# Kernel tuning notes

Hardware: AMD Instinct MI355X
Metric: run time of the kernel (lower is better)

Reference implementation:

```python
import jax, jax.numpy as jnp
import numpy as np

D_MODEL = 512
NHEAD = 8
HEAD_DIM = D_MODEL // NHEAD
D_FF = 2048
EPS = 1e-5


def _linear_params(key, d_in, d_out):
    kw, kb = jax.random.split(key)
    bound = 1.0 / np.sqrt(d_in)
    W = jax.random.uniform(kw, (d_out, d_in), jnp.float32, -bound, bound)
    b = jax.random.uniform(kb, (d_out,), jnp.float32, -bound, bound)
    return W, b


def setup_inputs() -> dict:
    key = jax.random.key(0)
    ks = jax.random.split(key, 8)
    src = jax.random.normal(ks[0], (4, 2048, D_MODEL), jnp.float32)
    Wq, bq = _linear_params(ks[1], D_MODEL, D_MODEL)
    Wk, bk = _linear_params(ks[2], D_MODEL, D_MODEL)
    Wv, bv = _linear_params(ks[3], D_MODEL, D_MODEL)
    Wo, bo = _linear_params(ks[4], D_MODEL, D_MODEL)
    W1, b1 = _linear_params(ks[5], D_MODEL, D_FF)
    W2, b2 = _linear_params(ks[6], D_FF, D_MODEL)
    g1 = jnp.ones((D_MODEL,), jnp.float32)
    be1 = jnp.zeros((D_MODEL,), jnp.float32)
    g2 = jnp.ones((D_MODEL,), jnp.float32)
    be2 = jnp.zeros((D_MODEL,), jnp.float32)
    return dict(src=src, Wq=Wq, bq=bq, Wk=Wk, bk=bk, Wv=Wv, bv=bv,
                Wo=Wo, bo=bo, W1=W1, b1=b1, W2=W2, b2=b2,
                g1=g1, be1=be1, g2=g2, be2=be2)


def _layer_norm(x, g, b):
    mu = jnp.mean(x, axis=-1, keepdims=True)
    var = jnp.mean(jnp.square(x - mu), axis=-1, keepdims=True)
    return (x - mu) / jnp.sqrt(var + EPS) * g + b


def reference(src, Wq, bq, Wk, bk, Wv, bv, Wo, bo, W1, b1, W2, b2, g1, be1, g2, be2):
    B, T, D = src.shape
    scale = np.sqrt(HEAD_DIM).astype(np.float32)
    # Projections (torch Linear: x @ W.T + b)
    Q = (src @ Wq.T + bq).reshape(B, T, NHEAD, HEAD_DIM).transpose(0, 2, 1, 3)
    K = (src @ Wk.T + bk).reshape(B, T, NHEAD, HEAD_DIM).transpose(0, 2, 1, 3)
    V = (src @ Wv.T + bv).reshape(B, T, NHEAD, HEAD_DIM).transpose(0, 2, 1, 3)
    # Explicit QK^T -> softmax -> V (no mask, dropout=0)
    scores = jnp.einsum('bhqd,bhkd->bhqk', Q, K) / scale  # (B,H,T,T)
    attn = jax.nn.softmax(scores, axis=-1)
    ctx = jnp.einsum('bhqk,bhkd->bhqd', attn, V)
    ctx = ctx.transpose(0, 2, 1, 3).reshape(B, T, D)
    attn_out = ctx @ Wo.T + bo
    # Add & Norm 1
    x = _layer_norm(src + attn_out, g1, be1)
    # FFN: Linear -> GELU -> Linear
    h = jax.nn.gelu(x @ W1.T + b1, approximate=False)
    ffn_out = h @ W2.T + b2
    # Add & Norm 2
    return _layer_norm(x + ffn_out, g2, be2)
```

## Files before the change

### kernel.cpp

```cpp
#include <hip/hip_runtime.h>
#include <hip/hip_bf16.h>
#include <hip/hip_fp16.h>
#include <math.h>

typedef __bf16 bf16_t;
typedef __bf16 bf16x8 __attribute__((ext_vector_type(8)));
typedef __bf16 bf16x2 __attribute__((ext_vector_type(2)));
typedef float  f32x4  __attribute__((ext_vector_type(4)));

#define D_MODEL 512
#define NHEAD   8
#define HD      64
#define D_FF    2048
#define TOKENS  8192
#define SEQ     2048
#define BATCH   4

__device__ __forceinline__ void gload16(const bf16_t* g, bf16_t* l)
{
    __builtin_amdgcn_global_load_lds(
        (const __attribute__((address_space(1))) void*)g,
        (__attribute__((address_space(3))) void*)l,
        16, 0, 0);
}

__device__ __forceinline__ void cvt4(const float* s, bf16_t* d)
{
    float4 v = *(const float4*)s;
    alignas(8) bf16_t t[4] = {(bf16_t)v.x, (bf16_t)v.y, (bf16_t)v.z, (bf16_t)v.w};
    *(uint2*)d = *(const uint2*)t;
}

__device__ __forceinline__ void barrier_raw() { asm volatile("s_barrier" ::: "memory"); }
__device__ __forceinline__ void sched_fence() { __builtin_amdgcn_sched_barrier(0); }

__device__ __forceinline__ float gelu_f(float x)
{
    const float y = fabsf(x) * 0.70710678118654752f;
    const float t = 1.0f / fmaf(0.3275911f, y, 1.0f);
    float p = fmaf(1.061405429f, t, -1.453152027f);
    p = fmaf(p, t, 1.421413741f);
    p = fmaf(p, t, -0.284496736f);
    p = fmaf(p, t, 0.254829592f);
    p *= t;
    const float e = __builtin_amdgcn_exp2f(-y * y * 1.4426950408889634f);
    float erfv = 1.0f - p * e;
    erfv = (x < 0.f) ? -erfv : erfv;
    return 0.5f * x * (1.0f + erfv);
}

__global__ void cvt_weights(const float* __restrict__ src,
                            const float* __restrict__ Wq, const float* __restrict__ Wk,
                            const float* __restrict__ Wv, const float* __restrict__ Wo,
                            const float* __restrict__ W1, const float* __restrict__ W2,
                            const float* __restrict__ bq, const float* __restrict__ bk,
                            const float* __restrict__ bv,
                            bf16_t* __restrict__ Xb,
                            bf16_t* __restrict__ Wqkvb, bf16_t* __restrict__ Wob,
                            bf16_t* __restrict__ W1b, bf16_t* __restrict__ W2b,
                            float* __restrict__ bqkv, float* __restrict__ zbias)
{
    int i = blockIdx.x * 256 + threadIdx.x;
    if (i < 1048576) { cvt4(src + (size_t)i * 4, Xb + (size_t)i * 4); return; }
    i -= 1048576;
    if (i < 65536)        cvt4(Wq + (size_t)i * 4,            Wqkvb + (size_t)i * 4);
    else if (i < 131072)  cvt4(Wk + (size_t)(i - 65536) * 4,  Wqkvb + (size_t)i * 4);
    else if (i < 196608)  cvt4(Wv + (size_t)(i - 131072) * 4, Wqkvb + (size_t)i * 4);
    else if (i < 262144)  cvt4(Wo + (size_t)(i - 196608) * 4, Wob + (size_t)(i - 196608) * 4);
    else if (i < 524288)  cvt4(W1 + (size_t)(i - 262144) * 4, W1b + (size_t)(i - 262144) * 4);
    else if (i < 786432)  cvt4(W2 + (size_t)(i - 524288) * 4, W2b + (size_t)(i - 524288) * 4);
    else if (i < 786816) {
        int j = i - 786432;
        const float* s = (j < 128) ? bq + j * 4 : (j < 256) ? bk + (j - 128) * 4
                                                            : bv + (j - 256) * 4;
        *(float4*)(bqkv + (j & 127) * 4 + (j >> 7) * 512) = *(const float4*)s;
    } else if (i < 786944) {
        int j = i - 786816;
        *(float4*)(zbias + j * 4) = make_float4(0.f, 0.f, 0.f, 0.f);
    }
}

template <int EPI>
__global__ __launch_bounds__(512, 2)
void gemm256(const bf16_t* __restrict__ A, const bf16_t* __restrict__ B,
             const float* __restrict__ bias, bf16_t* __restrict__ C,
             int M, int N, int K)
{
    __shared__ bf16_t sA[2][256][64];
    __shared__ bf16_t sB[2][256][64];
    bf16_t* sAf = &sA[0][0][0];
    bf16_t* sBf = &sB[0][0][0];

    const int tid  = threadIdx.x;
    const int wave = tid >> 6;
    const int lane = tid & 63;
    const int g    = lane >> 4;
    const int c16  = lane & 15;
    const int wm   = (wave >> 2) * 128;
    const int wn   = (wave & 3) * 64;

    const int nwg  = gridDim.x * gridDim.y;
    const int flat = blockIdx.y * gridDim.x + blockIdx.x;
    const int swz  = (flat & 7) * (nwg >> 3) + (flat >> 3);
    const int m0   = (swz / gridDim.x) * 256;
    const int n0   = (swz % gridDim.x) * 256;

    const f32x4 fz = {0.f, 0.f, 0.f, 0.f};
    f32x4 acc[8][4];
#pragma unroll
    for (int i = 0; i < 8; i++)
#pragma unroll
        for (int j = 0; j < 4; j++) acc[i][j] = fz;

    const bf16_t* gA[4]; const bf16_t* gB[4]; int fa[4];
#pragma unroll
    for (int i = 0; i < 4; i++) {
        const int f = i * 512 + tid, row = f >> 3, l = (f & 7) ^ (row & 7);
        fa[i] = f;
        gA[i] = A + (size_t)(m0 + row) * K + l * 8;
        gB[i] = B + (size_t)(n0 + row) * K + l * 8;
    }

    auto stage = [&](int ko, int buf) {
        bf16_t* dA = sAf + buf * (256 * 64);
        bf16_t* dB = sBf + buf * (256 * 64);
#pragma unroll
        for (int i = 0; i < 4; i++) gload16(gA[i] + ko, dA + fa[i] * 8);
#pragma unroll
        for (int i = 0; i < 4; i++) gload16(gB[i] + ko, dB + fa[i] * 8);
    };

    stage(0, 0);
    stage(64, 1);

    const int NS = K >> 6;
    for (int s = 0; s < NS; ++s) {
        const int cur = s & 1;
        if (s + 1 < NS) asm volatile("s_waitcnt vmcnt(8)" ::: "memory");
        else            asm volatile("s_waitcnt vmcnt(0)" ::: "memory");
        barrier_raw();
        sched_fence();

#pragma unroll
        for (int ks = 0; ks < 2; ++ks) {
            const int ck = ((ks * 4 + g) ^ (c16 & 7)) * 8;
            bf16x8 af[8], bfr[4];
#pragma unroll
            for (int i = 0; i < 8; i++)
                af[i] = *(const bf16x8*)&sA[cur][wm + i * 16 + c16][ck];
#pragma unroll
            for (int j = 0; j < 4; j++)
                bfr[j] = *(const bf16x8*)&sB[cur][wn + j * 16 + c16][ck];
#pragma unroll
            for (int mi = 0; mi < 8; mi++)
#pragma unroll
                for (int ni = 0; ni < 4; ni++)
                    acc[mi][ni] = __builtin_amdgcn_mfma_f32_16x16x32_bf16(
                        af[mi], bfr[ni], acc[mi][ni], 0, 0, 0);
        }

        sched_fence();
        barrier_raw();
        if (s + 2 < NS) stage((s + 2) << 6, cur);
        sched_fence();
    }

    float bcol[4];
#pragma unroll
    for (int ni = 0; ni < 4; ni++) bcol[ni] = bias[n0 + wn + ni * 16 + c16];
#pragma unroll
    for (int mi = 0; mi < 8; mi++) {
#pragma unroll
        for (int ni = 0; ni < 4; ni++) {
            const int col = n0 + wn + ni * 16 + c16;
#pragma unroll
            for (int r = 0; r < 4; r++) {
                const int row = m0 + wm + mi * 16 + g * 4 + r;
                float v = acc[mi][ni][r] + bcol[ni];
                if (EPI == 1) v = gelu_f(v);
                C[(size_t)row * N + col] = (bf16_t)v;
            }
        }
    }
}

template <int BM, int EPI, bool SPLIT2>
__global__ __launch_bounds__(256)
void gemm_bt(const bf16_t* __restrict__ A, const bf16_t* __restrict__ B,
             const float* __restrict__ bias, const float* __restrict__ biasz,
             void* __restrict__ Cout, int M, int N, int K)
{
    constexpr int MI = BM / 32;
    constexpr int NA = BM / 32;
    __shared__ bf16_t sA[2][BM][64];
    __shared__ bf16_t sB[2][128][64];
    bf16_t* sAf = &sA[0][0][0];
    bf16_t* sBf = &sB[0][0][0];

    const int tid  = threadIdx.x;
    const int wave = tid >> 6;
    const int lane = tid & 63;
    const int g    = lane >> 4;
    const int c16  = lane & 15;
    const int wm   = (wave >> 1) * (BM / 2);
    const int wn   = (wave & 1) * 64;
    const int m0   = blockIdx.y * BM;
    const int n0   = blockIdx.x * 128;

    const int zz    = SPLIT2 ? blockIdx.z : 0;
    const int Keff  = SPLIT2 ? (K >> 1) : K;
    const int kbase = zz * Keff;
    const float* bptr = (SPLIT2 && zz) ? biasz : bias;

    const f32x4 fz = {0.f, 0.f, 0.f, 0.f};
    f32x4 acc[MI][4];
#pragma unroll
    for (int i = 0; i < MI; i++)
#pragma unroll
        for (int j = 0; j < 4; j++) acc[i][j] = fz;

    const bf16_t* gA[NA]; int fa[NA];
#pragma unroll
    for (int i = 0; i < NA; i++) {
        const int f = i * 256 + tid, row = f >> 3, l = (f & 7) ^ (row & 7);
        fa[i] = f;
        gA[i] = A + (size_t)(m0 + row) * K + kbase + l * 8;
    }
    const bf16_t* gB[4]; int fb[4];
#pragma unroll
    for (int i = 0; i < 4; i++) {
        const int f = i * 256 + tid, row = f >> 3, l = (f & 7) ^ (row & 7);
        fb[i] = f;
        gB[i] = B + (size_t)(n0 + row) * K + kbase + l * 8;
    }

    auto stage = [&](int ko, int buf) {
        bf16_t* dA = sAf + buf * (BM * 64);
        bf16_t* dB = sBf + buf * 8192;
#pragma unroll
        for (int i = 0; i < NA; i++) gload16(gA[i] + ko, dA + fa[i] * 8);
#pragma unroll
        for (int i = 0; i < 4; i++)  gload16(gB[i] + ko, dB + fb[i] * 8);
    };

    stage(0, 0);
    stage(64, 1);

    const int NS = Keff >> 6;
    for (int s = 0; s < NS; ++s) {
        const int cur = s & 1;
        if (s + 1 < NS) {
            if constexpr (NA == 2) asm volatile("s_waitcnt vmcnt(6)" ::: "memory");
            else                   asm volatile("s_waitcnt vmcnt(8)" ::: "memory");
        } else {
            asm volatile("s_waitcnt vmcnt(0)" ::: "memory");
        }
        barrier_raw();
        sched_fence();

#pragma unroll
        for (int sub = 0; sub < 2; ++sub) {
            const int ck = (((sub * 4 + g) ^ (c16 & 7))) * 8;
            bf16x8 af[MI], bfr[4];
#pragma unroll
            for (int i = 0; i < MI; i++)
                af[i] = *(const bf16x8*)&sA[cur][wm + i * 16 + c16][ck];
#pragma unroll
            for (int j = 0; j < 4; j++)
                bfr[j] = *(const bf16x8*)&sB[cur][wn + j * 16 + c16][ck];
#pragma unroll
            for (int mi = 0; mi < MI; mi++)
#pragma unroll
                for (int ni = 0; ni < 4; ni++)
                    acc[mi][ni] = __builtin_amdgcn_mfma_f32_16x16x32_bf16(
                        af[mi], bfr[ni], acc[mi][ni], 0, 0, 0);
        }

        sched_fence();
        barrier_raw();
        if (s + 2 < NS) stage((s + 2) << 6, cur);
        sched_fence();
    }

    __half* outh = (__half*)Cout + (size_t)zz * M * N;
#pragma unroll
    for (int mi = 0; mi < MI; mi++) {
#pragma unroll
        for (int ni = 0; ni < 4; ni++) {
            const int col = n0 + wn + ni * 16 + c16;
            const float bv = bptr[col];
#pragma unroll
            for (int r = 0; r < 4; r++) {
                const int row = m0 + wm + mi * 16 + g * 4 + r;
                float v = acc[mi][ni][r] + bv;
                if (EPI == 1) v = gelu_f(v);
                if (EPI == 2)
                    outh[(size_t)row * N + col] = (__half)v;
                else
                    ((bf16_t*)Cout)[(size_t)row * N + col] = (bf16_t)v;
            }
        }
    }
}

__global__ __launch_bounds__(256)
void transpose_v(const bf16_t* __restrict__ qkv, bf16_t* __restrict__ vt)
{
    __shared__ bf16_t st[64][72];
    const int t0 = blockIdx.x * 64;
    const int bh = blockIdx.y;
    const int b = bh >> 3, h = bh & 7;
    const int tid = threadIdx.x;

    for (int c = tid; c < 512; c += 256) {
        int r = c >> 3, cj = (c & 7) * 8;
        const bf16_t* src = qkv + ((size_t)(b * SEQ + t0 + r)) * 1536 + 1024 + h * 64 + cj;
        *(int4*)&st[r][cj] = *(const int4*)src;
    }
    __syncthreads();
    for (int c = tid; c < 512; c += 256) {
        int d = c >> 3, pj = (c & 7) * 8;
        alignas(16) bf16_t tmp[8];
#pragma unroll
        for (int j = 0; j < 8; j++) {
            int p = pj + j;
            int t = ((p >> 5) << 5) + (((p >> 2) & 1) << 4) + (((p >> 3) & 3) << 2) + (p & 3);
            tmp[j] = st[t][d];
        }
        *(int4*)(vt + ((size_t)(bh * 64 + d)) * SEQ + t0 + pj) = *(const int4*)tmp;
    }
}

__global__ __launch_bounds__(512)
__attribute__((amdgpu_waves_per_eu(6)))
void flash_attn(const bf16_t* __restrict__ qkv, const bf16_t* __restrict__ vt,
                bf16_t* __restrict__ ctx)
{
    __shared__ bf16_t sK[3][64][64];
    __shared__ bf16_t sVt[3][64][64];

    const int bh = blockIdx.y;
    const int b = bh >> 3, h = bh & 7;
    const int q0 = blockIdx.x * 128;
    const int tid = threadIdx.x;
    const int wave = tid >> 6, lane = tid & 63;
    const int g = lane >> 4, c16 = lane & 15;

    const float qscale = 0.125f * 1.4426950408889634f;
    bf16x8 aq[2];
#pragma unroll
    for (int ks = 0; ks < 2; ks++) {
        bf16x8 v = *(const bf16x8*)(qkv +
            ((size_t)(b * SEQ + q0 + wave * 16 + c16)) * 1536 +
            h * 64 + ks * 32 + g * 8);
#pragma unroll
        for (int j = 0; j < 8; j++) v[j] = (bf16_t)((float)v[j] * qscale);
        aq[ks] = v;
    }

    const f32x4 fz = {0.f, 0.f, 0.f, 0.f};
    f32x4 acc_oT[4];
#pragma unroll
    for (int dt = 0; dt < 4; dt++) acc_oT[dt] = fz;
    float l_acc = 0.f;

    const int f0 = tid, r0 = f0 >> 3, l0 = (f0 & 7) ^ (r0 & 7);
    const bf16_t* gK0 = qkv + ((size_t)(b * SEQ + r0)) * 1536 + 512 + h * 64 + l0 * 8;
    const bf16_t* gV0 = vt + ((size_t)(bh * 64 + r0)) * SEQ + l0 * 8;
    bf16_t* lK = &sK[0][0][0];
    bf16_t* lV = &sVt[0][0][0];

    auto stageKV = [&](int t) {
        const int bo = (t % 3) * 4096;
        const size_t kv = (size_t)t * 64;
        gload16(gK0 + kv * 1536, lK + bo + f0 * 8);
        gload16(gV0 + kv,        lV + bo + f0 * 8);
    };

    f32x4 accs[4];
    auto qk_mfma = [&](int cur) {
#pragma unroll
        for (int tt = 0; tt < 4; tt++) accs[tt] = fz;
#pragma unroll
        for (int ks = 0; ks < 2; ks++) {
            const int pc = ((ks * 4 + g) ^ (c16 & 7)) * 8;
#pragma unroll
            for (int tt = 0; tt < 4; tt++) {
                bf16x8 ak = *(const bf16x8*)&sK[cur][tt * 16 + c16][pc];
                accs[tt] = __builtin_amdgcn_mfma_f32_16x16x32_bf16(ak, aq[ks], accs[tt], 0, 0, 0);
            }
        }
    };

    bf16x8 pb[2];
    auto pv_mfma = [&](int cur) {
#pragma unroll
        for (int kv = 0; kv < 2; kv++) {
            const int pc = ((kv * 4 + g) ^ (c16 & 7)) * 8;
#pragma unroll
            for (int dt = 0; dt < 4; dt++) {
                bf16x8 av = *(const bf16x8*)&sVt[cur][dt * 16 + c16][pc];
                acc_oT[dt] = __builtin_amdgcn_mfma_f32_16x16x32_bf16(av, pb[kv], acc_oT[dt], 0, 0, 0);
            }
        }
    };

    auto softmax_pack = [&]() {
#pragma unroll
        for (int tt = 0; tt < 4; tt++) {
            float s = 0.f;
#pragma unroll
            for (int r = 0; r < 4; r++) {
                float p = __builtin_amdgcn_exp2f(accs[tt][r]);
                accs[tt][r] = p;
                s += p;
            }
            l_acc += s;
        }
#pragma unroll
        for (int kv = 0; kv < 2; kv++)
#pragma unroll
            for (int j = 0; j < 8; j++)
                pb[kv][j] = (bf16_t)accs[kv * 2 + (j >> 2)][j & 3];
    };

    stageKV(0);
    stageKV(1);

    for (int it = 0; it < 32; ++it) {
        const int cur = it % 3;
        if (it < 31) asm volatile("s_waitcnt vmcnt(2)" ::: "memory");
        else         asm volatile("s_waitcnt vmcnt(0)" ::: "memory");
        barrier_raw();

        __builtin_amdgcn_s_setprio(1);
        qk_mfma(cur);
        __builtin_amdgcn_s_setprio(0);
        softmax_pack();
        __builtin_amdgcn_s_setprio(1);
        pv_mfma(cur);
        __builtin_amdgcn_s_setprio(0);

        if (it + 2 < 32) stageKV(it + 2);
    }

    {
        float l = l_acc;
        l += __shfl_xor(l, 16);
        l += __shfl_xor(l, 32);
        const float inv = 1.0f / l;
        const int token = q0 + wave * 16 + c16;
        bf16_t* dst = ctx + ((size_t)(b * SEQ + token)) * 512 + h * 64 + g * 4;
#pragma unroll
        for (int dt = 0; dt < 4; dt++) {
            alignas(8) bf16_t o4[4];
#pragma unroll
            for (int r = 0; r < 4; r++) o4[r] = (bf16_t)(acc_oT[dt][r] * inv);
            *(uint2*)(dst + dt * 16) = *(const uint2*)o4;
        }
    }
}

__global__ __launch_bounds__(256)
void add_ln3(const float* __restrict__ a, const __half* __restrict__ b,
             const __half* __restrict__ c,
             const float* __restrict__ gamma, const float* __restrict__ beta,
             float* __restrict__ outf, bf16_t* __restrict__ outb)
{
    const int row  = blockIdx.x * 4 + (threadIdx.x >> 6);
    const int lane = threadIdx.x & 63;
    const size_t base = (size_t)row * 512 + lane * 8;

    int4 braw = *(const int4*)(b + base);
    int4 craw = *(const int4*)(c + base);
    const __half* bh = (const __half*)&braw;
    const __half* ch = (const __half*)&craw;

    float v[8];
#pragma unroll
    for (int hh = 0; hh < 2; hh++) {
        float4 av = *(const float4*)(a + base + hh * 4);
        v[hh * 4 + 0] = av.x + (float)bh[hh * 4 + 0] + (float)ch[hh * 4 + 0];
        v[hh * 4 + 1] = av.y + (float)bh[hh * 4 + 1] + (float)ch[hh * 4 + 1];
        v[hh * 4 + 2] = av.z + (float)bh[hh * 4 + 2] + (float)ch[hh * 4 + 2];
        v[hh * 4 + 3] = av.w + (float)bh[hh * 4 + 3] + (float)ch[hh * 4 + 3];
    }

    float s = 0.f;
#pragma unroll
    for (int i = 0; i < 8; i++) s += v[i];
#pragma unroll
    for (int off = 32; off > 0; off >>= 1) s += __shfl_xor(s, off);
    const float mu = s * (1.f / 512.f);

    float q = 0.f;
#pragma unroll
    for (int i = 0; i < 8; i++) { float d = v[i] - mu; q += d * d; }
#pragma unroll
    for (int off = 32; off > 0; off >>= 1) q += __shfl_xor(q, off);
    const float rstd = rsqrtf(q * (1.f / 512.f) + 1e-5f);

    float4 g0 = *(const float4*)(gamma + lane * 8);
    float4 g1 = *(const float4*)(gamma + lane * 8 + 4);
    float4 e0 = *(const float4*)(beta + lane * 8);
    float4 e1 = *(const float4*)(beta + lane * 8 + 4);
    const float gg[8] = {g0.x, g0.y, g0.z, g0.w, g1.x, g1.y, g1.z, g1.w};
    const float ee[8] = {e0.x, e0.y, e0.z, e0.w, e1.x, e1.y, e1.z, e1.w};

    float o[8];
#pragma unroll
    for (int i = 0; i < 8; i++) o[i] = (v[i] - mu) * rstd * gg[i] + ee[i];

    *(float4*)(outf + base)     = make_float4(o[0], o[1], o[2], o[3]);
    *(float4*)(outf + base + 4) = make_float4(o[4], o[5], o[6], o[7]);
    if (outb) {
        alignas(16) bf16_t ob[8];
#pragma unroll
        for (int i = 0; i < 8; i++) ob[i] = (bf16_t)o[i];
        *(int4*)(outb + base) = *(const int4*)ob;
    }
}

extern "C" void kernel_launch(void* const* d_in, const int* in_sizes, int n_in,
                              void* d_out, int out_size, void* d_ws, size_t ws_size,
                              hipStream_t stream)
{
    const float* src = (const float*)d_in[0];
    const float* Wq  = (const float*)d_in[1];  const float* bq  = (const float*)d_in[2];
    const float* Wk  = (const float*)d_in[3];  const float* bk  = (const float*)d_in[4];
    const float* Wv  = (const float*)d_in[5];  const float* bv  = (const float*)d_in[6];
    const float* Wo  = (const float*)d_in[7];  const float* bo  = (const float*)d_in[8];
    const float* W1  = (const float*)d_in[9];  const float* b1  = (const float*)d_in[10];
    const float* W2  = (const float*)d_in[11]; const float* b2  = (const float*)d_in[12];
    const float* g1  = (const float*)d_in[13]; const float* be1 = (const float*)d_in[14];
    const float* g2  = (const float*)d_in[15]; const float* be2 = (const float*)d_in[16];
    float* out = (float*)d_out;

    char* ws = (char*)d_ws;
    size_t off = 0;
    auto alloc = [&](size_t bytes) -> void* {
        void* p = ws + off;
        off = (off + bytes + 255) & ~(size_t)255;
        return p;
    };

    bf16_t* Xb    = (bf16_t*)alloc((size_t)TOKENS * 512 * 2);
    bf16_t* Wqkvb = (bf16_t*)alloc((size_t)1536 * 512 * 2);
    bf16_t* Wob   = (bf16_t*)alloc((size_t)512 * 512 * 2);
    bf16_t* W1b   = (bf16_t*)alloc((size_t)2048 * 512 * 2);
    bf16_t* W2b   = (bf16_t*)alloc((size_t)512 * 2048 * 2);
    float*  bqkv  = (float*)alloc(1536 * 4);
    float*  zbias = (float*)alloc(512 * 4);
    bf16_t* QKV   = (bf16_t*)alloc((size_t)TOKENS * 1536 * 2);
    bf16_t* Vt    = (bf16_t*)alloc((size_t)32 * 64 * SEQ * 2);
    bf16_t* CTX   = (bf16_t*)alloc((size_t)TOKENS * 512 * 2);
    __half* ATTa  = (__half*)alloc((size_t)TOKENS * 512 * 2);
    __half* ATTb  = (__half*)alloc((size_t)TOKENS * 512 * 2);
    float*  X1    = (float*)alloc((size_t)TOKENS * 512 * 4);
    bf16_t* X1b   = (bf16_t*)alloc((size_t)TOKENS * 512 * 2);

    bf16_t* H    = QKV;
    __half* FFNa = ATTa;
    __half* FFNb = ATTb;

    cvt_weights<<<7170, 256, 0, stream>>>(src, Wq, Wk, Wv, Wo, W1, W2, bq, bk, bv,
                                          Xb, Wqkvb, Wob, W1b, W2b, bqkv, zbias);

    gemm256<0><<<dim3(6, 32), 512, 0, stream>>>(
        Xb, Wqkvb, bqkv, QKV, TOKENS, 1536, 512);

    transpose_v<<<dim3(32, 32), 256, 0, stream>>>(QKV, Vt);
    flash_attn<<<dim3(16, 32), 512, 0, stream>>>(QKV, Vt, CTX);

    gemm_bt<64, 2, true><<<dim3(4, 128, 2), 256, 0, stream>>>(
        CTX, Wob, bo, zbias, ATTa, TOKENS, 512, 512);

    add_ln3<<<2048, 256, 0, stream>>>(src, ATTa, ATTb, g1, be1, X1, X1b);

    gemm_bt<128, 1, false><<<dim3(16, 64), 256, 0, stream>>>(
        X1b, W1b, b1, zbias, H, TOKENS, 2048, 512);

    gemm_bt<64, 2, true><<<dim3(4, 128, 2), 256, 0, stream>>>(
        H, W2b, b2, zbias, FFNa, TOKENS, 512, 2048);

    add_ln3<<<2048, 256, 0, stream>>>(X1, FFNa, FFNb, g2, be2, out, nullptr);
}
```

Before: 269.5 us.

## Fuse V transpose into QKV GEMM epilogue and drop 256-tile GEMM

The QKV projection now runs through the generic 128x128 gemm_bt kernel with a new epilogue mode. In that mode, V columns are written directly into the permuted, transposed Vt layout that flash attention expects. This removes the separate transpose_v kernel launch and its extra read and write of V. In exchange, the dedicated 256x256 gemm256 kernel is dropped, and the V stores become scattered 2-byte writes strided by SEQ, which may coalesce poorly.

```diff
diff --git a/kernel.cpp b/kernel.cpp
--- a/kernel.cpp
+++ b/kernel.cpp
@@ -80,115 +80,12 @@
     }
 }
 
-template <int EPI>
-__global__ __launch_bounds__(512, 2)
-void gemm256(const bf16_t* __restrict__ A, const bf16_t* __restrict__ B,
-             const float* __restrict__ bias, bf16_t* __restrict__ C,
-             int M, int N, int K)
-{
-    __shared__ bf16_t sA[2][256][64];
-    __shared__ bf16_t sB[2][256][64];
-    bf16_t* sAf = &sA[0][0][0];
-    bf16_t* sBf = &sB[0][0][0];
-
-    const int tid  = threadIdx.x;
-    const int wave = tid >> 6;
-    const int lane = tid & 63;
-    const int g    = lane >> 4;
-    const int c16  = lane & 15;
-    const int wm   = (wave >> 2) * 128;
-    const int wn   = (wave & 3) * 64;
-
-    const int nwg  = gridDim.x * gridDim.y;
-    const int flat = blockIdx.y * gridDim.x + blockIdx.x;
-    const int swz  = (flat & 7) * (nwg >> 3) + (flat >> 3);
-    const int m0   = (swz / gridDim.x) * 256;
-    const int n0   = (swz % gridDim.x) * 256;
-
-    const f32x4 fz = {0.f, 0.f, 0.f, 0.f};
-    f32x4 acc[8][4];
-#pragma unroll
-    for (int i = 0; i < 8; i++)
-#pragma unroll
-        for (int j = 0; j < 4; j++) acc[i][j] = fz;
-
-    const bf16_t* gA[4]; const bf16_t* gB[4]; int fa[4];
-#pragma unroll
-    for (int i = 0; i < 4; i++) {
-        const int f = i * 512 + tid, row = f >> 3, l = (f & 7) ^ (row & 7);
-        fa[i] = f;
-        gA[i] = A + (size_t)(m0 + row) * K + l * 8;
-        gB[i] = B + (size_t)(n0 + row) * K + l * 8;
-    }
-
-    auto stage = [&](int ko, int buf) {
-        bf16_t* dA = sAf + buf * (256 * 64);
-        bf16_t* dB = sBf + buf * (256 * 64);
-#pragma unroll
-        for (int i = 0; i < 4; i++) gload16(gA[i] + ko, dA + fa[i] * 8);
-#pragma unroll
-        for (int i = 0; i < 4; i++) gload16(gB[i] + ko, dB + fa[i] * 8);
-    };
-
-    stage(0, 0);
-    stage(64, 1);
-
-    const int NS = K >> 6;
-    for (int s = 0; s < NS; ++s) {
-        const int cur = s & 1;
-        if (s + 1 < NS) asm volatile("s_waitcnt vmcnt(8)" ::: "memory");
-        else            asm volatile("s_waitcnt vmcnt(0)" ::: "memory");
-        barrier_raw();
-        sched_fence();
-
-#pragma unroll
-        for (int ks = 0; ks < 2; ++ks) {
-            const int ck = ((ks * 4 + g) ^ (c16 & 7)) * 8;
-            bf16x8 af[8], bfr[4];
-#pragma unroll
-            for (int i = 0; i < 8; i++)
-                af[i] = *(const bf16x8*)&sA[cur][wm + i * 16 + c16][ck];
-#pragma unroll
-            for (int j = 0; j < 4; j++)
-                bfr[j] = *(const bf16x8*)&sB[cur][wn + j * 16 + c16][ck];
-#pragma unroll
-            for (int mi = 0; mi < 8; mi++)
-#pragma unroll
-                for (int ni = 0; ni < 4; ni++)
-                    acc[mi][ni] = __builtin_amdgcn_mfma_f32_16x16x32_bf16(
-                        af[mi], bfr[ni], acc[mi][ni], 0, 0, 0);
-        }
-
-        sched_fence();
-        barrier_raw();
-        if (s + 2 < NS) stage((s + 2) << 6, cur);
-        sched_fence();
-    }
-
-    float bcol[4];
-#pragma unroll
-    for (int ni = 0; ni < 4; ni++) bcol[ni] = bias[n0 + wn + ni * 16 + c16];
-#pragma unroll
-    for (int mi = 0; mi < 8; mi++) {
-#pragma unroll
-        for (int ni = 0; ni < 4; ni++) {
-            const int col = n0 + wn + ni * 16 + c16;
-#pragma unroll
-            for (int r = 0; r < 4; r++) {
-                const int row = m0 + wm + mi * 16 + g * 4 + r;
-                float v = acc[mi][ni][r] + bcol[ni];
-                if (EPI == 1) v = gelu_f(v);
-                C[(size_t)row * N + col] = (bf16_t)v;
-            }
-        }
-    }
-}
-
 template <int BM, int EPI, bool SPLIT2>
 __global__ __launch_bounds__(256)
 void gemm_bt(const bf16_t* __restrict__ A, const bf16_t* __restrict__ B,
              const float* __restrict__ bias, const float* __restrict__ biasz,
-             void* __restrict__ Cout, int M, int N, int K)
+             void* __restrict__ Cout, bf16_t* __restrict__ vt,
+             int M, int N, int K)
 {
     constexpr int MI = BM / 32;
     constexpr int NA = BM / 32;
@@ -294,40 +191,25 @@
                 const int row = m0 + wm + mi * 16 + g * 4 + r;
                 float v = acc[mi][ni][r] + bv;
                 if (EPI == 1) v = gelu_f(v);
-                if (EPI == 2)
+                if (EPI == 2) {
                     outh[(size_t)row * N + col] = (__half)v;
-                else
+                } else if (EPI == 3 && col >= 1024) {
+                    const int c1 = col - 1024;
+                    const int h = c1 >> 6, d = c1 & 63;
+                    const int b = row >> 11;
+                    const int ts = row & 2047;
+                    const int tile = ts >> 6, w = ts & 63;
+                    const int p = (w & 0x23)
+                                | ((w & 0x08) << 1)
+                                | ((w & 0x04) << 1)
+                                | ((w & 0x10) >> 2);
+                    vt[((size_t)((b * 8 + h) * 64 + d)) * SEQ + tile * 64 + p] =
+                        (bf16_t)v;
+                } else {
                     ((bf16_t*)Cout)[(size_t)row * N + col] = (bf16_t)v;
+                }
             }
         }
-    }
-}
-
-__global__ __launch_bounds__(256)
-void transpose_v(const bf16_t* __restrict__ qkv, bf16_t* __restrict__ vt)
-{
-    __shared__ bf16_t st[64][72];
-    const int t0 = blockIdx.x * 64;
-    const int bh = blockIdx.y;
-    const int b = bh >> 3, h = bh & 7;
-    const int tid = threadIdx.x;
-
-    for (int c = tid; c < 512; c += 256) {
-        int r = c >> 3, cj = (c & 7) * 8;
-        const bf16_t* src = qkv + ((size_t)(b * SEQ + t0 + r)) * 1536 + 1024 + h * 64 + cj;
-        *(int4*)&st[r][cj] = *(const int4*)src;
-    }
-    __syncthreads();
-    for (int c = tid; c < 512; c += 256) {
-        int d = c >> 3, pj = (c & 7) * 8;
-        alignas(16) bf16_t tmp[8];
-#pragma unroll
-        for (int j = 0; j < 8; j++) {
-            int p = pj + j;
-            int t = ((p >> 5) << 5) + (((p >> 2) & 1) << 4) + (((p >> 3) & 3) << 2) + (p & 3);
-            tmp[j] = st[t][d];
-        }
-        *(int4*)(vt + ((size_t)(bh * 64 + d)) * SEQ + t0 + pj) = *(const int4*)tmp;
     }
 }
 
@@ -566,22 +448,21 @@
     cvt_weights<<<7170, 256, 0, stream>>>(src, Wq, Wk, Wv, Wo, W1, W2, bq, bk, bv,
                                           Xb, Wqkvb, Wob, W1b, W2b, bqkv, zbias);
 
-    gemm256<0><<<dim3(6, 32), 512, 0, stream>>>(
-        Xb, Wqkvb, bqkv, QKV, TOKENS, 1536, 512);
-
-    transpose_v<<<dim3(32, 32), 256, 0, stream>>>(QKV, Vt);
+    gemm_bt<128, 3, false><<<dim3(12, 64), 256, 0, stream>>>(
+        Xb, Wqkvb, bqkv, zbias, QKV, Vt, TOKENS, 1536, 512);
+
     flash_attn<<<dim3(16, 32), 512, 0, stream>>>(QKV, Vt, CTX);
 
     gemm_bt<64, 2, true><<<dim3(4, 128, 2), 256, 0, stream>>>(
-        CTX, Wob, bo, zbias, ATTa, TOKENS, 512, 512);
+        CTX, Wob, bo, zbias, ATTa, nullptr, TOKENS, 512, 512);
 
     add_ln3<<<2048, 256, 0, stream>>>(src, ATTa, ATTb, g1, be1, X1, X1b);
 
     gemm_bt<128, 1, false><<<dim3(16, 64), 256, 0, stream>>>(
-        X1b, W1b, b1, zbias, H, TOKENS, 2048, 512);
+        X1b, W1b, b1, zbias, H, nullptr, TOKENS, 2048, 512);
 
     gemm_bt<64, 2, true><<<dim3(4, 128, 2), 256, 0, stream>>>(
-        H, W2b, b2, zbias, FFNa, TOKENS, 512, 2048);
+        H, W2b, b2, zbias, FFNa, nullptr, TOKENS, 512, 2048);
 
     add_ln3<<<2048, 256, 0, stream>>>(X1, FFNa, FFNb, g2, be2, out, nullptr);
 }
```

Measured after the change: 282.8 us. 1.05x slower.
